# Kernel optimization log

Hardware: AMD Instinct MI355X
Metric: run time of the kernel (lower is better)

Reference implementation:

```python
import jax, jax.numpy as jnp
import numpy as np

N_NODES = 50000
N_EDGES = 1_600_000
REL_NUM = 16
D_IN = 64
D_OUT = 64


def setup_inputs() -> dict:
    key = jax.random.key(0)
    k_h, k_w, k_n, k_s, k_d, k_r = jax.random.split(key, 6)
    h = jax.random.normal(k_h, (N_NODES, D_IN), dtype=jnp.float32)
    # xavier_uniform over (rel_num, input_dim, output_dim): fan_in=input_dim, fan_out=output_dim
    limit = float(np.sqrt(6.0 / (D_IN + D_OUT)))
    weight = jax.random.uniform(k_w, (REL_NUM, D_IN, D_OUT), dtype=jnp.float32,
                                minval=-limit, maxval=limit)
    norm = jax.random.uniform(k_n, (N_EDGES, 1), dtype=jnp.float32)
    src = jax.random.randint(k_s, (N_EDGES,), 0, N_NODES)
    dst = jax.random.randint(k_d, (N_EDGES,), 0, N_NODES)
    rel_type = jax.random.randint(k_r, (N_EDGES,), 0, REL_NUM)
    return {"h": h, "weight": weight, "norm": norm,
            "src": src, "dst": dst, "rel_type": rel_type}


def reference(h, weight, norm, src, dst, rel_type):
    # Non-input path of R_GCN_Layer:
    #   msg_e = (h[src_e] @ weight[rel_e]) * norm_e ; h'_v = relu(sum_{e->v} msg_e)
    # Instead of gathering a [E, D_in, D_out] weight tensor per edge (huge),
    # transform every node by every relation once, then gather per (src, rel).
    n_nodes = h.shape[0]
    transformed = jnp.einsum('nd,rdo->nro', h, weight)      # [N, R, D_out]
    msg = transformed[src, rel_type] * norm                  # [E, D_out]
    agg = jax.ops.segment_sum(msg, dst, num_segments=n_nodes)  # [N, D_out]
    return jax.nn.relu(agg)
```

## Files before the change

kernel.cpp:

```cpp
#include <hip/hip_runtime.h>
#include <hip/hip_bf16.h>

#define N_NODES 50000
#define N_EDGES 1600000
#define NREL    16
#define DIM     64

#define BKT_SZ  16
#define NTILE   3125
#define NSEG_AL 50049

#define CB_SH   7
#define NCB     391
#define P1_CHUNK 2048
#define P1_GRID  782

#define CB_R_ARENA 5120
#define CB_ARENA 8704
#define EMAX    (NCB * CB_ARENA)
#define PREP_HBLK 3125

typedef __attribute__((ext_vector_type(8))) short short8;
typedef __attribute__((ext_vector_type(4))) float float4v;
typedef __attribute__((ext_vector_type(4))) unsigned short ushort4v;

template<int IS_F32>
__device__ __forceinline__ float ldx(const void* p, size_t i) {
    if (IS_F32) {
        return ((const float*)p)[i];
    } else {
        unsigned short u = ((const unsigned short*)p)[i];
        return __uint_as_float(((unsigned)u) << 16);
    }
}

__device__ __forceinline__ float bfbits2f(unsigned short u) {
    return __uint_as_float(((unsigned)u) << 16);
}

__device__ __forceinline__ unsigned short f2bfbits(float v) {
    __hip_bfloat16 b = __float2bfloat16(v);
    unsigned short us; __builtin_memcpy(&us, &b, 2);
    return us;
}

__global__ __launch_bounds__(1024) void k_detect(
    const float* __restrict__ norm_f, int* __restrict__ flag,
    int* __restrict__ gcur)
{
    __shared__ int sbad;
    if (threadIdx.x == 0) sbad = 0;
    if (threadIdx.x < NCB) gcur[threadIdx.x] = 0;
    __syncthreads();
    float v = norm_f[threadIdx.x];
    int bad = (v != v || fabsf(v) > 1e3f) ? 1 : 0;
    if (bad) atomicOr(&sbad, 1);
    __syncthreads();
    if (threadIdx.x == 0) *flag = sbad ? 0 : 1;
}

template<int IS_F32>
__device__ __forceinline__ void split_body(
    const int* __restrict__ src, const int* __restrict__ dst,
    const int* __restrict__ rel, const void* __restrict__ norm_raw,
    int* __restrict__ gcur, unsigned long long* __restrict__ R,
    int* hist, int* curs)
{
    const int blk = blockIdx.x;
    for (int i = threadIdx.x; i < NCB; i += 256) hist[i] = 0;
    __syncthreads();
    const int e0 = blk * P1_CHUNK;
    for (int i = threadIdx.x; i < P1_CHUNK; i += 256) {
        int e = e0 + i;
        if (e < N_EDGES) atomicAdd(&hist[dst[e] >> CB_SH], 1);
    }
    __syncthreads();
    for (int b = threadIdx.x; b < NCB; b += 256) {
        int c = hist[b];
        if (c > 0) {
            int s = atomicAdd(&gcur[b], c);
            if (s + c > CB_R_ARENA) s = CB_R_ARENA - c;
            curs[b] = b * CB_R_ARENA + s;
        }
    }
    __syncthreads();
    for (int i = threadIdx.x; i < P1_CHUNK; i += 256) {
        int e = e0 + i;
        if (e >= N_EDGES) continue;
        int d = dst[e];
        int pos = atomicAdd(&curs[d >> CB_SH], 1);
        unsigned short nb = f2bfbits(ldx<IS_F32>(norm_raw, e));
        unsigned long long rec =
              (unsigned long long)(d & 127)
            | ((unsigned long long)(unsigned)src[e] << 8)
            | ((unsigned long long)(unsigned)rel[e] << 24)
            | ((unsigned long long)nb << 32);
        R[pos] = rec;
    }
}

__global__ __launch_bounds__(256) void k_split_prep(
    const int* __restrict__ src, const int* __restrict__ dst,
    const int* __restrict__ rel, const void* __restrict__ norm_raw,
    int* __restrict__ gcur, unsigned long long* __restrict__ R,
    const void* __restrict__ h_raw, const void* __restrict__ w_raw,
    unsigned short* __restrict__ hbf, unsigned short* __restrict__ Wswz,
    const int* __restrict__ flag)
{
    __shared__ int hist[NCB];
    __shared__ int curs[NCB];
    const int blk = blockIdx.x;
    if (blk < P1_GRID) {
        if (*flag) split_body<1>(src, dst, rel, norm_raw, gcur, R, hist, curs);
        else       split_body<0>(src, dst, rel, norm_raw, gcur, R, hist, curs);
    } else {
        const int f = *flag;
        const int blk2 = blk - P1_GRID;
        if (blk2 < PREP_HBLK) {
            const int x = threadIdx.x & 15, rl = threadIdx.x >> 4;
            const int row = blk2 * 16 + rl;
            const size_t rb = (size_t)row * 64;
            ushort4v o;
            if (f) {
                const float* hf = (const float*)h_raw;
                o[0] = f2bfbits(hf[rb + x]);
                o[1] = f2bfbits(hf[rb + x + 16]);
                o[2] = f2bfbits(hf[rb + x + 32]);
                o[3] = f2bfbits(hf[rb + x + 48]);
            } else {
                const unsigned short* hr = (const unsigned short*)h_raw;
                o[0] = hr[rb + x];
                o[1] = hr[rb + x + 16];
                o[2] = hr[rb + x + 32];
                o[3] = hr[rb + x + 48];
            }
            *(ushort4v*)(hbf + rb + 4 * x) = o;
        } else {
            int rel2 = blk2 - PREP_HBLK;
            for (int idx = threadIdx.x; idx < 4096; idx += 256) {
                int d = idx >> 6, o = idx & 63;
                float wv = f ? ((const float*)w_raw)[(size_t)((rel2 << 6) + d) * 64 + o]
                             : bfbits2f(((const unsigned short*)w_raw)[(size_t)((rel2 << 6) + d) * 64 + o]);
                int c = d >> 5, q = (d >> 3) & 3, j = d & 7;
                Wswz[(size_t)rel2 * 5120 + ((c << 6) + o) * 40 + q * 8 + j] = f2bfbits(wv);
            }
        }
    }
}

__global__ __launch_bounds__(256) void k_fine(
    const int* __restrict__ gcur,
    const unsigned long long* __restrict__ R,
    unsigned* __restrict__ packed2, unsigned short* __restrict__ normS,
    int* __restrict__ segBase, int* __restrict__ segCnt)
{
    __shared__ int cnt[128], sbl[128], curs[128];
    const int tid = threadIdx.x, cb = blockIdx.x;
    if (tid < 128) { cnt[tid] = 0; curs[tid] = 0; }
    __syncthreads();
    const int c0 = cb * CB_R_ARENA;
    const int c1 = c0 + min(gcur[cb], CB_R_ARENA);

    for (int i = c0 + tid; i < c1; i += 256) {
        unsigned long long rec = R[i];
        int bin = (int)((rec >> 24) & 15) * 8 + (int)((rec >> 4) & 7);
        atomicAdd(&cnt[bin], 1);
    }
    __syncthreads();

    if (tid == 0) {
        int g = cb * CB_ARENA;
        for (int j = 0; j < 128; ++j) {
            sbl[j] = g;
            g += (cnt[j] + 31) & ~31;
        }
    }
    __syncthreads();

    if (tid < 128) {
        int seg = ((cb * 8 + (tid & 7)) << 4) + (tid >> 3);
        segBase[seg] = sbl[tid];
        segCnt[seg]  = cnt[tid];
    }

    for (int i = c0 + tid; i < c1; i += 256) {
        unsigned long long rec = R[i];
        int bin = (int)((rec >> 24) & 15) * 8 + (int)((rec >> 4) & 7);
        int pos = sbl[bin] + atomicAdd(&curs[bin], 1);
        packed2[pos] = (unsigned)rec & 0x00FFFF0Fu;
        normS[pos]   = (unsigned short)(rec >> 32);
    }
    __syncthreads();

    for (int p = tid; p < 128 * 32; p += 256) {
        int bin = p >> 5, j = p & 31;
        int c = cnt[bin], pe = (c + 31) & ~31;
        if (j < pe - c) {
            int pos = sbl[bin] + c + j;
            packed2[pos] = 0;
            normS[pos]   = 0;
        }
    }
}

#define MFMA_BF16 __builtin_amdgcn_mfma_f32_16x16x32_bf16

__global__ __launch_bounds__(256) void k_fused2(
    const unsigned* __restrict__ packed2,
    const unsigned short* __restrict__ normS,
    const unsigned short* __restrict__ hbf,
    const unsigned short* __restrict__ Wswz,
    const int* __restrict__ segBase,
    const int* __restrict__ segCnt,
    void* __restrict__ out, const int* __restrict__ flag)
{
    __shared__ __align__(16) unsigned short sbuf[4][16 * 72];
    __shared__ float pbuf[2][64][17];
    const int tid  = threadIdx.x;
    const int lane = tid & 63, wave = tid >> 6;
    const int n15  = lane & 15, quad = lane >> 4;
    const int tin  = wave >> 1;
    const int half = wave & 1;
    const int tile = blockIdx.x * 2 + tin;
    const bool valid = (tile < NTILE);

    float4v ac0 = {0.f,0.f,0.f,0.f}, ac1 = {0.f,0.f,0.f,0.f};
    float4v ac2 = {0.f,0.f,0.f,0.f}, ac3 = {0.f,0.f,0.f,0.f};
    unsigned short* sb_ = &sbuf[wave][0];

    if (valid) {
        const int r0 = half * 8;
        for (int r = r0; r < r0 + 8; ++r) {
            const int sgb  = segBase[tile * 16 + r];
            const int scnt = segCnt[tile * 16 + r];
            if (scnt == 0) continue;
            const int nch = (scnt + 31) >> 5;

            float4v s0 = {0.f,0.f,0.f,0.f}, s1 = {0.f,0.f,0.f,0.f};
            float4v s2 = {0.f,0.f,0.f,0.f}, s3 = {0.f,0.f,0.f,0.f};

            for (int c = 0; c < nch; ++c) {
                const int e0 = sgb + (c << 5) + (quad << 3);
                const uint4 pa = *(const uint4*)(packed2 + e0);
                const uint4 pb = *(const uint4*)(packed2 + e0 + 4);
                const ushort4v na = *(const ushort4v*)(normS + e0);
                const ushort4v nb = *(const ushort4v*)(normS + e0 + 4);

                const int co = 4 * n15;
                ushort4v v0 = *(const ushort4v*)(hbf + (size_t)(pa.x >> 8) * 64 + co);
                ushort4v v1 = *(const ushort4v*)(hbf + (size_t)(pa.y >> 8) * 64 + co);
                ushort4v v2 = *(const ushort4v*)(hbf + (size_t)(pa.z >> 8) * 64 + co);
                ushort4v v3 = *(const ushort4v*)(hbf + (size_t)(pa.w >> 8) * 64 + co);
                ushort4v v4 = *(const ushort4v*)(hbf + (size_t)(pb.x >> 8) * 64 + co);
                ushort4v v5 = *(const ushort4v*)(hbf + (size_t)(pb.y >> 8) * 64 + co);
                ushort4v v6 = *(const ushort4v*)(hbf + (size_t)(pb.z >> 8) * 64 + co);
                ushort4v v7 = *(const ushort4v*)(hbf + (size_t)(pb.w >> 8) * 64 + co);

                short8 av;
                av[0] = ((int)(pa.x & 15u) == n15) ? (short)na[0] : (short)0;
                av[1] = ((int)(pa.y & 15u) == n15) ? (short)na[1] : (short)0;
                av[2] = ((int)(pa.z & 15u) == n15) ? (short)na[2] : (short)0;
                av[3] = ((int)(pa.w & 15u) == n15) ? (short)na[3] : (short)0;
                av[4] = ((int)(pb.x & 15u) == n15) ? (short)nb[0] : (short)0;
                av[5] = ((int)(pb.y & 15u) == n15) ? (short)nb[1] : (short)0;
                av[6] = ((int)(pb.z & 15u) == n15) ? (short)nb[2] : (short)0;
                av[7] = ((int)(pb.w & 15u) == n15) ? (short)nb[3] : (short)0;

#define BV_MFMA(S, K) \
                { short8 bv; \
                  bv[0] = (short)v0[K]; bv[1] = (short)v1[K]; \
                  bv[2] = (short)v2[K]; bv[3] = (short)v3[K]; \
                  bv[4] = (short)v4[K]; bv[5] = (short)v5[K]; \
                  bv[6] = (short)v6[K]; bv[7] = (short)v7[K]; \
                  S = MFMA_BF16(av, bv, S, 0, 0, 0); }

                BV_MFMA(s0, 0)
                BV_MFMA(s1, 1)
                BV_MFMA(s2, 2)
                BV_MFMA(s3, 3)
#undef BV_MFMA
            }

#pragma unroll
            for (int i = 0; i < 4; ++i) {
                sb_[(quad * 4 + i) * 72 +  0 + n15] = f2bfbits(s0[i]);
                sb_[(quad * 4 + i) * 72 + 16 + n15] = f2bfbits(s1[i]);
                sb_[(quad * 4 + i) * 72 + 32 + n15] = f2bfbits(s2[i]);
                sb_[(quad * 4 + i) * 72 + 48 + n15] = f2bfbits(s3[i]);
            }

            const short8 a0 = *(const short8*)(sb_ + n15 * 72 + quad * 8);
            const short8 a1 = *(const short8*)(sb_ + n15 * 72 + 32 + quad * 8);

            const unsigned short* wp = Wswz + (size_t)r * 5120;
            const short8 w00 = *(const short8*)(wp + ( 0 + n15) * 40 + quad * 8);
            const short8 w01 = *(const short8*)(wp + (16 + n15) * 40 + quad * 8);
            const short8 w02 = *(const short8*)(wp + (32 + n15) * 40 + quad * 8);
            const short8 w03 = *(const short8*)(wp + (48 + n15) * 40 + quad * 8);
            const short8 w10 = *(const short8*)(wp + (64 + n15) * 40 + quad * 8);
            const short8 w11 = *(const short8*)(wp + (80 + n15) * 40 + quad * 8);
            const short8 w12 = *(const short8*)(wp + (96 + n15) * 40 + quad * 8);
            const short8 w13 = *(const short8*)(wp + (112 + n15) * 40 + quad * 8);

            ac0 = MFMA_BF16(a0, w00, ac0, 0, 0, 0);
            ac1 = MFMA_BF16(a0, w01, ac1, 0, 0, 0);
            ac2 = MFMA_BF16(a0, w02, ac2, 0, 0, 0);
            ac3 = MFMA_BF16(a0, w03, ac3, 0, 0, 0);
            ac0 = MFMA_BF16(a1, w10, ac0, 0, 0, 0);
            ac1 = MFMA_BF16(a1, w11, ac1, 0, 0, 0);
            ac2 = MFMA_BF16(a1, w12, ac2, 0, 0, 0);
            ac3 = MFMA_BF16(a1, w13, ac3, 0, 0, 0);
        }
    }

    if (half) {
#pragma unroll
        for (int i = 0; i < 4; ++i) {
            pbuf[tin][lane][i]      = ac0[i];
            pbuf[tin][lane][4 + i]  = ac1[i];
            pbuf[tin][lane][8 + i]  = ac2[i];
            pbuf[tin][lane][12 + i] = ac3[i];
        }
    }
    __syncthreads();
    if (!half && valid) {
#pragma unroll
        for (int i = 0; i < 4; ++i) {
            ac0[i] += pbuf[tin][lane][i];
            ac1[i] += pbuf[tin][lane][4 + i];
            ac2[i] += pbuf[tin][lane][8 + i];
            ac3[i] += pbuf[tin][lane][12 + i];
        }
        const int node0 = tile << 4;
        const int f = *flag;
#define STORE_T(AC, T) \
        { \
            _Pragma("unroll") \
            for (int i = 0; i < 4; ++i) { \
                float rv = fmaxf(AC[i], 0.f); \
                size_t ob = (size_t)(node0 + quad * 4 + i) * 64 + (T) * 16 + n15; \
                if (f) ((float*)out)[ob] = rv; \
                else   ((unsigned short*)out)[ob] = f2bfbits(rv); \
            } \
        }
        STORE_T(ac0, 0)
        STORE_T(ac1, 1)
        STORE_T(ac2, 2)
        STORE_T(ac3, 3)
#undef STORE_T
    }
}

extern "C" void kernel_launch(void* const* d_in, const int* in_sizes, int n_in,
                              void* d_out, int out_size, void* d_ws, size_t ws_size,
                              hipStream_t stream)
{
    const void* h      = d_in[0];
    const void* weight = d_in[1];
    const void* norm   = d_in[2];
    const int* src = (const int*)d_in[3];
    const int* dst = (const int*)d_in[4];
    const int* rel = (const int*)d_in[5];

    char* w = (char*)d_ws;
    int* flag = (int*)w;                        w += 256;
    int* gcur = (int*)w;                        w += (NCB * 4 + 255) / 256 * 256;
    int* segBase = (int*)w;                     w += ((size_t)NSEG_AL * 4 + 255) / 256 * 256;
    int* segCnt  = (int*)w;                     w += ((size_t)NSEG_AL * 4 + 255) / 256 * 256;
    unsigned long long* R = (unsigned long long*)w;  w += (size_t)NCB * CB_R_ARENA * 8;
    unsigned* packed2 = (unsigned*)w;           w += ((size_t)EMAX * 4 + 255) / 256 * 256;
    unsigned short* normS = (unsigned short*)w; w += ((size_t)EMAX * 2 + 255) / 256 * 256;
    unsigned short* hbf = (unsigned short*)w;   w += (size_t)N_NODES * DIM * 2;
    unsigned short* Wswz = (unsigned short*)w;  w += (size_t)NREL * 5120 * 2;

    k_detect<<<1, 1024, 0, stream>>>((const float*)norm, flag, gcur);

    k_split_prep<<<P1_GRID + PREP_HBLK + NREL, 256, 0, stream>>>(
        src, dst, rel, norm, gcur, R, h, weight, hbf, Wswz, flag);

    k_fine<<<NCB, 256, 0, stream>>>(gcur, R, packed2, normS, segBase, segCnt);

    k_fused2<<<(NTILE + 1) / 2, 256, 0, stream>>>(packed2, normS, hbf, Wswz,
                                                  segBase, segCnt, d_out, flag);
}
```

Measured before the change: 213.8 us.

## Fuse fine bucketing into aggregation kernel using shared-memory edge bins

Merges the fine-sort kernel and the MFMA aggregation kernel into one 512-thread kernel per coarse bucket. Edges are binned into shared memory (wave-shuffle prefix sum, padding to 8 with tail masking) instead of being written to global packed arrays and read back, which removes a launch plus a global write and read of the sorted edges. Each wave now owns one 16-node tile across all 16 relations, so the cross-wave reduction goes away. The cost is only 391 blocks with large LDS use, which lowers occupancy, and a possible LDS overflow if a bucket exceeds LBIN.

```diff
diff --git a/kernel.cpp b/kernel.cpp
--- a/kernel.cpp
+++ b/kernel.cpp
@@ -6,9 +6,7 @@
 #define NREL    16
 #define DIM     64
 
-#define BKT_SZ  16
 #define NTILE   3125
-#define NSEG_AL 50049
 
 #define CB_SH   7
 #define NCB     391
@@ -16,8 +14,7 @@
 #define P1_GRID  782
 
 #define CB_R_ARENA 5120
-#define CB_ARENA 8704
-#define EMAX    (NCB * CB_ARENA)
+#define LBIN    6080
 #define PREP_HBLK 3125
 
 typedef __attribute__((ext_vector_type(8))) short short8;
@@ -148,189 +145,169 @@
     }
 }
 
-__global__ __launch_bounds__(256) void k_fine(
+#define MFMA_BF16 __builtin_amdgcn_mfma_f32_16x16x32_bf16
+
+__global__ __launch_bounds__(512) void k_fuse3(
     const int* __restrict__ gcur,
     const unsigned long long* __restrict__ R,
-    unsigned* __restrict__ packed2, unsigned short* __restrict__ normS,
-    int* __restrict__ segBase, int* __restrict__ segCnt)
-{
-    __shared__ int cnt[128], sbl[128], curs[128];
+    const unsigned short* __restrict__ hbf,
+    const unsigned short* __restrict__ Wswz,
+    void* __restrict__ out, const int* __restrict__ flag)
+{
+    __shared__ unsigned pkL[LBIN];
+    __shared__ unsigned short nrmL[LBIN];
+    __shared__ int cnt[128], sbl[128], cur[128];
+    __shared__ int tot0s;
+    __shared__ __align__(16) unsigned short sbuf[8][16 * 72];
+
     const int tid = threadIdx.x, cb = blockIdx.x;
-    if (tid < 128) { cnt[tid] = 0; curs[tid] = 0; }
-    __syncthreads();
-    const int c0 = cb * CB_R_ARENA;
-    const int c1 = c0 + min(gcur[cb], CB_R_ARENA);
-
-    for (int i = c0 + tid; i < c1; i += 256) {
-        unsigned long long rec = R[i];
+    const int wave = tid >> 6, lane = tid & 63;
+    const int n15 = lane & 15, quad = lane >> 4;
+
+    if (tid < 128) { cnt[tid] = 0; cur[tid] = 0; }
+    __syncthreads();
+
+    const int c0  = cb * CB_R_ARENA;
+    const int run = min(gcur[cb], CB_R_ARENA);
+
+    for (int i = tid; i < run; i += 512) {
+        unsigned long long rec = R[c0 + i];
         int bin = (int)((rec >> 24) & 15) * 8 + (int)((rec >> 4) & 7);
         atomicAdd(&cnt[bin], 1);
     }
     __syncthreads();
 
-    if (tid == 0) {
-        int g = cb * CB_ARENA;
-        for (int j = 0; j < 128; ++j) {
-            sbl[j] = g;
-            g += (cnt[j] + 31) & ~31;
-        }
-    }
-    __syncthreads();
-
-    if (tid < 128) {
-        int seg = ((cb * 8 + (tid & 7)) << 4) + (tid >> 3);
-        segBase[seg] = sbl[tid];
-        segCnt[seg]  = cnt[tid];
-    }
-
-    for (int i = c0 + tid; i < c1; i += 256) {
-        unsigned long long rec = R[i];
+    if (tid < 64) {
+        int c = (cnt[tid] + 7) & ~7, incl = c;
+#pragma unroll
+        for (int off = 1; off < 64; off <<= 1) {
+            int t = __shfl_up(incl, off, 64);
+            if (tid >= off) incl += t;
+        }
+        sbl[tid] = incl - c;
+        if (tid == 63) tot0s = incl;
+    }
+    __syncthreads();
+    if (tid >= 64 && tid < 128) {
+        int l2 = tid - 64;
+        int c = (cnt[tid] + 7) & ~7, incl = c;
+#pragma unroll
+        for (int off = 1; off < 64; off <<= 1) {
+            int t = __shfl_up(incl, off, 64);
+            if (l2 >= off) incl += t;
+        }
+        sbl[tid] = tot0s + incl - c;
+    }
+    __syncthreads();
+
+    for (int i = tid; i < run; i += 512) {
+        unsigned long long rec = R[c0 + i];
         int bin = (int)((rec >> 24) & 15) * 8 + (int)((rec >> 4) & 7);
-        int pos = sbl[bin] + atomicAdd(&curs[bin], 1);
-        packed2[pos] = (unsigned)rec & 0x00FFFF0Fu;
-        normS[pos]   = (unsigned short)(rec >> 32);
-    }
-    __syncthreads();
-
-    for (int p = tid; p < 128 * 32; p += 256) {
-        int bin = p >> 5, j = p & 31;
-        int c = cnt[bin], pe = (c + 31) & ~31;
-        if (j < pe - c) {
-            int pos = sbl[bin] + c + j;
-            packed2[pos] = 0;
-            normS[pos]   = 0;
-        }
-    }
-}
-
-#define MFMA_BF16 __builtin_amdgcn_mfma_f32_16x16x32_bf16
-
-__global__ __launch_bounds__(256) void k_fused2(
-    const unsigned* __restrict__ packed2,
-    const unsigned short* __restrict__ normS,
-    const unsigned short* __restrict__ hbf,
-    const unsigned short* __restrict__ Wswz,
-    const int* __restrict__ segBase,
-    const int* __restrict__ segCnt,
-    void* __restrict__ out, const int* __restrict__ flag)
-{
-    __shared__ __align__(16) unsigned short sbuf[4][16 * 72];
-    __shared__ float pbuf[2][64][17];
-    const int tid  = threadIdx.x;
-    const int lane = tid & 63, wave = tid >> 6;
-    const int n15  = lane & 15, quad = lane >> 4;
-    const int tin  = wave >> 1;
-    const int half = wave & 1;
-    const int tile = blockIdx.x * 2 + tin;
-    const bool valid = (tile < NTILE);
+        int pos = sbl[bin] + atomicAdd(&cur[bin], 1);
+        pkL[pos]  = (unsigned)rec & 0x00FFFF0Fu;
+        nrmL[pos] = (unsigned short)(rec >> 32);
+    }
+    __syncthreads();
+
+    const int tile = cb * 8 + wave;
 
     float4v ac0 = {0.f,0.f,0.f,0.f}, ac1 = {0.f,0.f,0.f,0.f};
     float4v ac2 = {0.f,0.f,0.f,0.f}, ac3 = {0.f,0.f,0.f,0.f};
     unsigned short* sb_ = &sbuf[wave][0];
 
-    if (valid) {
-        const int r0 = half * 8;
-        for (int r = r0; r < r0 + 8; ++r) {
-            const int sgb  = segBase[tile * 16 + r];
-            const int scnt = segCnt[tile * 16 + r];
-            if (scnt == 0) continue;
-            const int nch = (scnt + 31) >> 5;
-
-            float4v s0 = {0.f,0.f,0.f,0.f}, s1 = {0.f,0.f,0.f,0.f};
-            float4v s2 = {0.f,0.f,0.f,0.f}, s3 = {0.f,0.f,0.f,0.f};
-
-            for (int c = 0; c < nch; ++c) {
-                const int e0 = sgb + (c << 5) + (quad << 3);
-                const uint4 pa = *(const uint4*)(packed2 + e0);
-                const uint4 pb = *(const uint4*)(packed2 + e0 + 4);
-                const ushort4v na = *(const ushort4v*)(normS + e0);
-                const ushort4v nb = *(const ushort4v*)(normS + e0 + 4);
-
-                const int co = 4 * n15;
-                ushort4v v0 = *(const ushort4v*)(hbf + (size_t)(pa.x >> 8) * 64 + co);
-                ushort4v v1 = *(const ushort4v*)(hbf + (size_t)(pa.y >> 8) * 64 + co);
-                ushort4v v2 = *(const ushort4v*)(hbf + (size_t)(pa.z >> 8) * 64 + co);
-                ushort4v v3 = *(const ushort4v*)(hbf + (size_t)(pa.w >> 8) * 64 + co);
-                ushort4v v4 = *(const ushort4v*)(hbf + (size_t)(pb.x >> 8) * 64 + co);
-                ushort4v v5 = *(const ushort4v*)(hbf + (size_t)(pb.y >> 8) * 64 + co);
-                ushort4v v6 = *(const ushort4v*)(hbf + (size_t)(pb.z >> 8) * 64 + co);
-                ushort4v v7 = *(const ushort4v*)(hbf + (size_t)(pb.w >> 8) * 64 + co);
-
-                short8 av;
-                av[0] = ((int)(pa.x & 15u) == n15) ? (short)na[0] : (short)0;
-                av[1] = ((int)(pa.y & 15u) == n15) ? (short)na[1] : (short)0;
-                av[2] = ((int)(pa.z & 15u) == n15) ? (short)na[2] : (short)0;
-                av[3] = ((int)(pa.w & 15u) == n15) ? (short)na[3] : (short)0;
-                av[4] = ((int)(pb.x & 15u) == n15) ? (short)nb[0] : (short)0;
-                av[5] = ((int)(pb.y & 15u) == n15) ? (short)nb[1] : (short)0;
-                av[6] = ((int)(pb.z & 15u) == n15) ? (short)nb[2] : (short)0;
-                av[7] = ((int)(pb.w & 15u) == n15) ? (short)nb[3] : (short)0;
+    for (int r = 0; r < NREL; ++r) {
+        const int bin = r * 8 + wave;
+        const int bb = sbl[bin], bc = cnt[bin];
+        if (bc == 0) continue;
+        const int nch = (bc + 31) >> 5;
+
+        float4v s0 = {0.f,0.f,0.f,0.f}, s1 = {0.f,0.f,0.f,0.f};
+        float4v s2 = {0.f,0.f,0.f,0.f}, s3 = {0.f,0.f,0.f,0.f};
+
+        for (int c = 0; c < nch; ++c) {
+            const int base = bb + (c << 5) + (quad << 3);
+            const int rem  = bc - ((c << 5) + (quad << 3));
+            const uint4 pa = *(const uint4*)&pkL[base];
+            const uint4 pb = *(const uint4*)&pkL[base + 4];
+            const ushort4v na = *(const ushort4v*)&nrmL[base];
+            const ushort4v nb = *(const ushort4v*)&nrmL[base + 4];
+
+            const unsigned r0s = (rem > 0) ? (pa.x >> 8) : 0u;
+            const unsigned r1s = (rem > 1) ? (pa.y >> 8) : 0u;
+            const unsigned r2s = (rem > 2) ? (pa.z >> 8) : 0u;
+            const unsigned r3s = (rem > 3) ? (pa.w >> 8) : 0u;
+            const unsigned r4s = (rem > 4) ? (pb.x >> 8) : 0u;
+            const unsigned r5s = (rem > 5) ? (pb.y >> 8) : 0u;
+            const unsigned r6s = (rem > 6) ? (pb.z >> 8) : 0u;
+            const unsigned r7s = (rem > 7) ? (pb.w >> 8) : 0u;
+
+            const int co = 4 * n15;
+            ushort4v v0 = *(const ushort4v*)(hbf + (size_t)r0s * 64 + co);
+            ushort4v v1 = *(const ushort4v*)(hbf + (size_t)r1s * 64 + co);
+            ushort4v v2 = *(const ushort4v*)(hbf + (size_t)r2s * 64 + co);
+            ushort4v v3 = *(const ushort4v*)(hbf + (size_t)r3s * 64 + co);
+            ushort4v v4 = *(const ushort4v*)(hbf + (size_t)r4s * 64 + co);
+            ushort4v v5 = *(const ushort4v*)(hbf + (size_t)r5s * 64 + co);
+            ushort4v v6 = *(const ushort4v*)(hbf + (size_t)r6s * 64 + co);
+            ushort4v v7 = *(const ushort4v*)(hbf + (size_t)r7s * 64 + co);
+
+            short8 av;
+            av[0] = (rem > 0 && (int)(pa.x & 15u) == n15) ? (short)na[0] : (short)0;
+            av[1] = (rem > 1 && (int)(pa.y & 15u) == n15) ? (short)na[1] : (short)0;
+            av[2] = (rem > 2 && (int)(pa.z & 15u) == n15) ? (short)na[2] : (short)0;
+            av[3] = (rem > 3 && (int)(pa.w & 15u) == n15) ? (short)na[3] : (short)0;
+            av[4] = (rem > 4 && (int)(pb.x & 15u) == n15) ? (short)nb[0] : (short)0;
+            av[5] = (rem > 5 && (int)(pb.y & 15u) == n15) ? (short)nb[1] : (short)0;
+            av[6] = (rem > 6 && (int)(pb.z & 15u) == n15) ? (short)nb[2] : (short)0;
+            av[7] = (rem > 7 && (int)(pb.w & 15u) == n15) ? (short)nb[3] : (short)0;
 
 #define BV_MFMA(S, K) \
-                { short8 bv; \
-                  bv[0] = (short)v0[K]; bv[1] = (short)v1[K]; \
-                  bv[2] = (short)v2[K]; bv[3] = (short)v3[K]; \
-                  bv[4] = (short)v4[K]; bv[5] = (short)v5[K]; \
-                  bv[6] = (short)v6[K]; bv[7] = (short)v7[K]; \
-                  S = MFMA_BF16(av, bv, S, 0, 0, 0); }
-
-                BV_MFMA(s0, 0)
-                BV_MFMA(s1, 1)
-                BV_MFMA(s2, 2)
-                BV_MFMA(s3, 3)
+            { short8 bv; \
+              bv[0] = (short)v0[K]; bv[1] = (short)v1[K]; \
+              bv[2] = (short)v2[K]; bv[3] = (short)v3[K]; \
+              bv[4] = (short)v4[K]; bv[5] = (short)v5[K]; \
+              bv[6] = (short)v6[K]; bv[7] = (short)v7[K]; \
+              S = MFMA_BF16(av, bv, S, 0, 0, 0); }
+
+            BV_MFMA(s0, 0)
+            BV_MFMA(s1, 1)
+            BV_MFMA(s2, 2)
+            BV_MFMA(s3, 3)
 #undef BV_MFMA
-            }
-
-#pragma unroll
-            for (int i = 0; i < 4; ++i) {
-                sb_[(quad * 4 + i) * 72 +  0 + n15] = f2bfbits(s0[i]);
-                sb_[(quad * 4 + i) * 72 + 16 + n15] = f2bfbits(s1[i]);
-                sb_[(quad * 4 + i) * 72 + 32 + n15] = f2bfbits(s2[i]);
-                sb_[(quad * 4 + i) * 72 + 48 + n15] = f2bfbits(s3[i]);
-            }
-
-            const short8 a0 = *(const short8*)(sb_ + n15 * 72 + quad * 8);
-            const short8 a1 = *(const short8*)(sb_ + n15 * 72 + 32 + quad * 8);
-
-            const unsigned short* wp = Wswz + (size_t)r * 5120;
-            const short8 w00 = *(const short8*)(wp + ( 0 + n15) * 40 + quad * 8);
-            const short8 w01 = *(const short8*)(wp + (16 + n15) * 40 + quad * 8);
-            const short8 w02 = *(const short8*)(wp + (32 + n15) * 40 + quad * 8);
-            const short8 w03 = *(const short8*)(wp + (48 + n15) * 40 + quad * 8);
-            const short8 w10 = *(const short8*)(wp + (64 + n15) * 40 + quad * 8);
-            const short8 w11 = *(const short8*)(wp + (80 + n15) * 40 + quad * 8);
-            const short8 w12 = *(const short8*)(wp + (96 + n15) * 40 + quad * 8);
-            const short8 w13 = *(const short8*)(wp + (112 + n15) * 40 + quad * 8);
-
-            ac0 = MFMA_BF16(a0, w00, ac0, 0, 0, 0);
-            ac1 = MFMA_BF16(a0, w01, ac1, 0, 0, 0);
-            ac2 = MFMA_BF16(a0, w02, ac2, 0, 0, 0);
-            ac3 = MFMA_BF16(a0, w03, ac3, 0, 0, 0);
-            ac0 = MFMA_BF16(a1, w10, ac0, 0, 0, 0);
-            ac1 = MFMA_BF16(a1, w11, ac1, 0, 0, 0);
-            ac2 = MFMA_BF16(a1, w12, ac2, 0, 0, 0);
-            ac3 = MFMA_BF16(a1, w13, ac3, 0, 0, 0);
-        }
-    }
-
-    if (half) {
+        }
+
 #pragma unroll
         for (int i = 0; i < 4; ++i) {
-            pbuf[tin][lane][i]      = ac0[i];
-            pbuf[tin][lane][4 + i]  = ac1[i];
-            pbuf[tin][lane][8 + i]  = ac2[i];
-            pbuf[tin][lane][12 + i] = ac3[i];
-        }
-    }
-    __syncthreads();
-    if (!half && valid) {
-#pragma unroll
-        for (int i = 0; i < 4; ++i) {
-            ac0[i] += pbuf[tin][lane][i];
-            ac1[i] += pbuf[tin][lane][4 + i];
-            ac2[i] += pbuf[tin][lane][8 + i];
-            ac3[i] += pbuf[tin][lane][12 + i];
-        }
+            sb_[(quad * 4 + i) * 72 +  0 + n15] = f2bfbits(s0[i]);
+            sb_[(quad * 4 + i) * 72 + 16 + n15] = f2bfbits(s1[i]);
+            sb_[(quad * 4 + i) * 72 + 32 + n15] = f2bfbits(s2[i]);
+            sb_[(quad * 4 + i) * 72 + 48 + n15] = f2bfbits(s3[i]);
+        }
+
+        const short8 a0 = *(const short8*)(sb_ + n15 * 72 + quad * 8);
+        const short8 a1 = *(const short8*)(sb_ + n15 * 72 + 32 + quad * 8);
+
+        const unsigned short* wp = Wswz + (size_t)r * 5120;
+        const short8 w00 = *(const short8*)(wp + ( 0 + n15) * 40 + quad * 8);
+        const short8 w01 = *(const short8*)(wp + (16 + n15) * 40 + quad * 8);
+        const short8 w02 = *(const short8*)(wp + (32 + n15) * 40 + quad * 8);
+        const short8 w03 = *(const short8*)(wp + (48 + n15) * 40 + quad * 8);
+        const short8 w10 = *(const short8*)(wp + (64 + n15) * 40 + quad * 8);
+        const short8 w11 = *(const short8*)(wp + (80 + n15) * 40 + quad * 8);
+        const short8 w12 = *(const short8*)(wp + (96 + n15) * 40 + quad * 8);
+        const short8 w13 = *(const short8*)(wp + (112 + n15) * 40 + quad * 8);
+
+        ac0 = MFMA_BF16(a0, w00, ac0, 0, 0, 0);
+        ac1 = MFMA_BF16(a0, w01, ac1, 0, 0, 0);
+        ac2 = MFMA_BF16(a0, w02, ac2, 0, 0, 0);
+        ac3 = MFMA_BF16(a0, w03, ac3, 0, 0, 0);
+        ac0 = MFMA_BF16(a1, w10, ac0, 0, 0, 0);
+        ac1 = MFMA_BF16(a1, w11, ac1, 0, 0, 0);
+        ac2 = MFMA_BF16(a1, w12, ac2, 0, 0, 0);
+        ac3 = MFMA_BF16(a1, w13, ac3, 0, 0, 0);
+    }
+
+    if (tile < NTILE) {
         const int node0 = tile << 4;
         const int f = *flag;
 #define STORE_T(AC, T) \
@@ -365,11 +342,7 @@
     char* w = (char*)d_ws;
     int* flag = (int*)w;                        w += 256;
     int* gcur = (int*)w;                        w += (NCB * 4 + 255) / 256 * 256;
-    int* segBase = (int*)w;                     w += ((size_t)NSEG_AL * 4 + 255) / 256 * 256;
-    int* segCnt  = (int*)w;                     w += ((size_t)NSEG_AL * 4 + 255) / 256 * 256;
     unsigned long long* R = (unsigned long long*)w;  w += (size_t)NCB * CB_R_ARENA * 8;
-    unsigned* packed2 = (unsigned*)w;           w += ((size_t)EMAX * 4 + 255) / 256 * 256;
-    unsigned short* normS = (unsigned short*)w; w += ((size_t)EMAX * 2 + 255) / 256 * 256;
     unsigned short* hbf = (unsigned short*)w;   w += (size_t)N_NODES * DIM * 2;
     unsigned short* Wswz = (unsigned short*)w;  w += (size_t)NREL * 5120 * 2;
 
@@ -378,8 +351,5 @@
     k_split_prep<<<P1_GRID + PREP_HBLK + NREL, 256, 0, stream>>>(
         src, dst, rel, norm, gcur, R, h, weight, hbf, Wswz, flag);
 
-    k_fine<<<NCB, 256, 0, stream>>>(gcur, R, packed2, normS, segBase, segCnt);
-
-    k_fused2<<<(NTILE + 1) / 2, 256, 0, stream>>>(packed2, normS, hbf, Wswz,
-                                                  segBase, segCnt, d_out, flag);
-}
+    k_fuse3<<<NCB, 512, 0, stream>>>(gcur, R, hbf, Wswz, d_out, flag);
+}
```

Result: faster. 180.3 us (-15.7%).
